# Kernel tuning notes

Measured on AMD Instinct MI355X. Metric: run time of the kernel, lower is better.

## Reference

```python
import jax, jax.numpy as jnp
import numpy as np

B, N, DIM = 1024, 256, 64
NFP, L = 10000, 3
EPS = 1e-6


def layer_norm(x, g, b):
    mu = jnp.mean(x, axis=-1, keepdims=True)
    var = jnp.mean(jnp.square(x - mu), axis=-1, keepdims=True)
    return (x - mu) * jax.lax.rsqrt(var + EPS) * g + b


def setup_inputs() -> dict:
    key = jax.random.key(0)
    ks = jax.random.split(key, 12)
    fingerprints = jax.random.randint(ks[0], (B, N), 0, NFP)
    # sparse-ish symmetric 0/1 adjacency mask (float, as in torch .mul)
    a = (jax.random.uniform(ks[1], (B, N, N)) < 0.05).astype(jnp.float32)
    adjacencies = jnp.maximum(a, jnp.swapaxes(a, 1, 2))
    molecular_sizes = jax.random.randint(ks[2], (B,), 1, N + 1)
    s = 0.02
    word_emb = jax.random.normal(ks[3], (NFP, DIM), jnp.float32) * s
    pos_emb = jax.random.normal(ks[4], (N, DIM), jnp.float32) * s
    emb_ln_g = jnp.ones((DIM,), jnp.float32)
    emb_ln_b = jnp.zeros((DIM,), jnp.float32)
    W1 = jax.random.normal(ks[5], (L, DIM, DIM), jnp.float32) * s
    b1 = jnp.zeros((L, DIM), jnp.float32)
    W2 = jax.random.normal(ks[6], (L, DIM, DIM), jnp.float32) * s
    b2 = jnp.zeros((L, DIM), jnp.float32)
    W3 = jax.random.normal(ks[7], (L, DIM, DIM), jnp.float32) * s
    b3 = jnp.zeros((L, DIM), jnp.float32)
    ln_g = jnp.ones((DIM,), jnp.float32)
    ln_b = jnp.zeros((DIM,), jnp.float32)
    return {"fingerprints": fingerprints, "adjacencies": adjacencies,
            "molecular_sizes": molecular_sizes, "word_emb": word_emb,
            "pos_emb": pos_emb, "emb_ln_g": emb_ln_g, "emb_ln_b": emb_ln_b,
            "W1": W1, "b1": b1, "W2": W2, "b2": b2, "W3": W3, "b3": b3,
            "ln_g": ln_g, "ln_b": ln_b}


def reference(fingerprints, adjacencies, molecular_sizes, word_emb, pos_emb,
              emb_ln_g, emb_ln_b, W1, b1, W2, b2, W3, b3, ln_g, ln_b):
    # demb: word + position embedding, LayerNorm (dropout = identity in eval)
    xs = word_emb[fingerprints] + pos_emb[None, :, :]        # [B, N, D]
    xs = layer_norm(xs, emb_ln_g, emb_ln_b)
    for l in range(L):
        hs1 = jax.nn.relu(jnp.einsum('bnd,ed->bne', xs, W1[l]) + b1[l])
        hs2 = jax.nn.relu(jnp.einsum('bnd,ed->bne', xs, W2[l]) + b2[l])
        attn = jnp.einsum('bnd,bmd->bnm', hs1, hs2) * adjacencies  # masked QK^T, no softmax
        hs3 = jax.nn.relu(jnp.einsum('bnd,ed->bne', xs, W3[l]) + b3[l])
        xs = xs + layer_norm(jnp.einsum('bnm,bmd->bnd', attn, hs3), ln_g, ln_b)
    return xs
```

## Files before the change

kernel.cpp:

```cpp
#include <hip/hip_runtime.h>


#define NB   1024
#define NN   256
#define DD   64
#define NLAY 3

typedef __attribute__((ext_vector_type(8))) short s16x8;
typedef __attribute__((ext_vector_type(4))) short s16x4;
typedef __attribute__((ext_vector_type(4))) float f32x4;

static __device__ __forceinline__ short f2bf(float x) {
    union { float f; unsigned u; } v; v.f = x;
    unsigned r = v.u + 0x7FFFu + ((v.u >> 16) & 1u);
    return (short)(r >> 16);
}

#define MFMA(a, bb, acc) __builtin_amdgcn_mfma_f32_16x16x32_bf16((a), (bb), (acc), 0, 0, 0)

#define STAGE_STRIP(arr)                                                      \
    do {                                                                      \
        _Pragma("unroll") for (int tr_ = 0; tr_ < 2; ++tr_)                   \
        _Pragma("unroll") for (int et_ = 0; et_ < 4; ++et_)                   \
        _Pragma("unroll") for (int r_ = 0; r_ < 4; ++r_)                      \
            hs2s[n0 + tr_*16 + g*4 + r_][et_*16 + c] = f2bf(arr[tr_][et_][r_]); \
    } while (0)

#define READ_AFRAG(dst)                                                       \
    do {                                                                      \
        _Pragma("unroll") for (int tr_ = 0; tr_ < 2; ++tr_)                   \
        _Pragma("unroll") for (int kb_ = 0; kb_ < 2; ++kb_)                   \
            dst[tr_][kb_] = *(const s16x8*)&hs2s[n0 + tr_*16 + c][kb_*32 + g*8]; \
    } while (0)

__global__ __launch_bounds__(512, 2)
void mgnn_fused(const int* __restrict__ fpr, const float* __restrict__ adj,
                const float* __restrict__ wemb, const float* __restrict__ pemb,
                const float* __restrict__ egp, const float* __restrict__ ebp,
                const float* __restrict__ W1p, const float* __restrict__ b1p,
                const float* __restrict__ W2p, const float* __restrict__ b2p,
                const float* __restrict__ W3p, const float* __restrict__ b3p,
                const float* __restrict__ lngp, const float* __restrict__ lnbp,
                float* __restrict__ out)
{
    __shared__ __align__(16) short hs2s[NN][72];
    __shared__ __align__(16) short hs3Ts[DD][264];

    const int b    = blockIdx.x;
    const int tid  = threadIdx.x;
    const int w    = tid >> 6;
    const int lane = tid & 63;
    const int g    = lane >> 4;
    const int c    = lane & 15;
    const int n0   = w * 32;

    const float* __restrict__ adjB = adj + (size_t)b * NN * NN;

    f32x4 xsC[2][4];
    #pragma unroll
    for (int tr = 0; tr < 2; ++tr) {
        const int n = n0 + tr*16 + c;
        const int f = fpr[b*NN + n];
        f32x4 v[4];
        float s1 = 0.f, s2 = 0.f;
        #pragma unroll
        for (int dc = 0; dc < 4; ++dc) {
            const f32x4 wv = *(const f32x4*)&wemb[f*DD + dc*16 + g*4];
            const f32x4 pe = *(const f32x4*)&pemb[n*DD + dc*16 + g*4];
            f32x4 t;
            #pragma unroll
            for (int r = 0; r < 4; ++r) {
                t[r] = wv[r] + pe[r]; s1 += t[r]; s2 += t[r]*t[r];
            }
            v[dc] = t;
        }
        s1 += __shfl_xor(s1, 16); s2 += __shfl_xor(s2, 16);
        s1 += __shfl_xor(s1, 32); s2 += __shfl_xor(s2, 32);
        const float mu  = s1 * 0.015625f;
        const float var = s2 * 0.015625f - mu*mu;
        const float rs  = rsqrtf(var + 1e-6f);
        #pragma unroll
        for (int dc = 0; dc < 4; ++dc) {
            const f32x4 eg = *(const f32x4*)&egp[dc*16 + g*4];
            const f32x4 eb = *(const f32x4*)&ebp[dc*16 + g*4];
            #pragma unroll
            for (int r = 0; r < 4; ++r)
                xsC[tr][dc][r] = (v[dc][r] - mu) * rs * eg[r] + eb[r];
        }
    }

    auto stageXS = [&]() {
        #pragma unroll
        for (int tr = 0; tr < 2; ++tr)
            #pragma unroll
            for (int dc = 0; dc < 4; ++dc) {
                s16x4 pk;
                #pragma unroll
                for (int r = 0; r < 4; ++r) pk[r] = f2bf(xsC[tr][dc][r]);
                *(s16x4*)&hs2s[n0 + tr*16 + c][dc*16 + g*4] = pk;
            }
    };

    s16x8 xsf[2][2];
    stageXS();
    __syncthreads();
    READ_AFRAG(xsf);

    float hsv[2][4][4];

    auto gemmHs = [&](const float* __restrict__ Wm, const float* __restrict__ bm) {
        s16x8 wf[4][2];
        #pragma unroll
        for (int et = 0; et < 4; ++et) {
            const float* p = Wm + (et*16 + c)*DD + g*8;
            #pragma unroll
            for (int kb = 0; kb < 2; ++kb) {
                s16x8 v;
                #pragma unroll
                for (int j = 0; j < 8; ++j) v[j] = f2bf(p[kb*32 + j]);
                wf[et][kb] = v;
            }
        }
        #pragma unroll
        for (int tr = 0; tr < 2; ++tr) {
            #pragma unroll
            for (int et = 0; et < 4; ++et) {
                f32x4 acc = {0.f, 0.f, 0.f, 0.f};
                acc = MFMA(xsf[tr][0], wf[et][0], acc);
                acc = MFMA(xsf[tr][1], wf[et][1], acc);
                const float bv = bm[et*16 + c];
                #pragma unroll
                for (int r = 0; r < 4; ++r)
                    hsv[tr][et][r] = fmaxf(acc[r] + bv, 0.f);
            }
        }
    };

    #pragma unroll 1
    for (int l = 0; l < NLAY; ++l) {
        gemmHs(W1p + l*DD*DD, b1p + l*DD);
        STAGE_STRIP(hsv);
        __syncthreads();
        s16x8 h1f[2][2];
        READ_AFRAG(h1f);

        gemmHs(W2p + l*DD*DD, b2p + l*DD);
        STAGE_STRIP(hsv);

        gemmHs(W3p + l*DD*DD, b3p + l*DD);
        #pragma unroll
        for (int tr = 0; tr < 2; ++tr) {
            #pragma unroll
            for (int et = 0; et < 4; ++et) {
                s16x4 pk;
                #pragma unroll
                for (int r = 0; r < 4; ++r) pk[r] = f2bf(hsv[tr][et][r]);
                *(s16x4*)&hs3Ts[et*16 + c][n0 + tr*16 + g*4] = pk;
            }
        }
        __syncthreads();

        f32x4 pv[2][4];
        {
            const f32x4 z4 = {0.f, 0.f, 0.f, 0.f};
            #pragma unroll
            for (int tr = 0; tr < 2; ++tr)
                #pragma unroll
                for (int dc = 0; dc < 4; ++dc) pv[tr][dc] = z4;
        }

        #pragma unroll 1
        for (int cc = 0; cc < 8; ++cc) {
            float amT[2][2][4];
            #pragma unroll
            for (int tr = 0; tr < 2; ++tr)
                #pragma unroll
                for (int mc = 0; mc < 2; ++mc)
                    #pragma unroll
                    for (int r = 0; r < 4; ++r)
                        amT[tr][mc][r] =
                            adjB[(size_t)(cc*32 + mc*16 + g*4 + r)*NN + n0 + tr*16 + c];

            s16x8 a2[2][2];
            #pragma unroll
            for (int mc = 0; mc < 2; ++mc)
                #pragma unroll
                for (int kb = 0; kb < 2; ++kb)
                    a2[mc][kb] = *(const s16x8*)&hs2s[cc*32 + mc*16 + c][kb*32 + g*8];

            s16x8 h3f[4];
            #pragma unroll
            for (int dc = 0; dc < 4; ++dc)
                h3f[dc] = *(const s16x8*)&hs3Ts[dc*16 + c][cc*32 + g*8];

            float smv[2][2][4];
            #pragma unroll
            for (int tr = 0; tr < 2; ++tr) {
                #pragma unroll
                for (int mc = 0; mc < 2; ++mc) {
                    f32x4 st = {0.f, 0.f, 0.f, 0.f};
                    st = MFMA(a2[mc][0], h1f[tr][0], st);
                    st = MFMA(a2[mc][1], h1f[tr][1], st);
                    #pragma unroll
                    for (int r = 0; r < 4; ++r)
                        smv[tr][mc][r] = st[r] * amT[tr][mc][r];
                }
            }

            #pragma unroll
            for (int tr = 0; tr < 2; ++tr) {
                s16x8 pb;
                #pragma unroll
                for (int j = 0; j < 8; ++j) {
                    const int srcl = ((2*(g & 1) + (j >> 2)) << 4) | c;
                    const float v0 = __shfl(smv[tr][0][j & 3], srcl);
                    const float v1 = __shfl(smv[tr][1][j & 3], srcl);
                    pb[j] = f2bf((g & 2) ? v1 : v0);
                }
                #pragma unroll
                for (int dc = 0; dc < 4; ++dc)
                    pv[tr][dc] = MFMA(h3f[dc], pb, pv[tr][dc]);
            }
        }

        #pragma unroll
        for (int tr = 0; tr < 2; ++tr) {
            float s1 = 0.f, s2 = 0.f;
            #pragma unroll
            for (int dc = 0; dc < 4; ++dc)
                #pragma unroll
                for (int r = 0; r < 4; ++r) {
                    const float x = pv[tr][dc][r];
                    s1 += x; s2 += x*x;
                }
            s1 += __shfl_xor(s1, 16); s2 += __shfl_xor(s2, 16);
            s1 += __shfl_xor(s1, 32); s2 += __shfl_xor(s2, 32);
            const float mu  = s1 * 0.015625f;
            const float var = s2 * 0.015625f - mu*mu;
            const float rs  = rsqrtf(var + 1e-6f);
            #pragma unroll
            for (int dc = 0; dc < 4; ++dc) {
                const f32x4 lg = *(const f32x4*)&lngp[dc*16 + g*4];
                const f32x4 lb = *(const f32x4*)&lnbp[dc*16 + g*4];
                #pragma unroll
                for (int r = 0; r < 4; ++r)
                    xsC[tr][dc][r] += (pv[tr][dc][r] - mu) * rs * lg[r] + lb[r];
            }
        }

        if (l < NLAY - 1) {
            __syncthreads();
            stageXS();
            __syncthreads();
            READ_AFRAG(xsf);
        }
    }

    const size_t ob = (size_t)b * NN * DD;
    #pragma unroll
    for (int tr = 0; tr < 2; ++tr) {
        const int n = n0 + tr*16 + c;
        #pragma unroll
        for (int dc = 0; dc < 4; ++dc)
            *(f32x4*)&out[ob + (size_t)n*DD + dc*16 + g*4] = xsC[tr][dc];
    }
}

extern "C" void kernel_launch(void* const* d_in, const int* in_sizes, int n_in,
                              void* d_out, int out_size, void* d_ws, size_t ws_size,
                              hipStream_t stream) {
    const int*   fpr  = (const int*)  d_in[0];
    const float* adj  = (const float*)d_in[1];
    const float* wemb = (const float*)d_in[3];
    const float* pemb = (const float*)d_in[4];
    const float* eg   = (const float*)d_in[5];
    const float* eb   = (const float*)d_in[6];
    const float* W1   = (const float*)d_in[7];
    const float* b1   = (const float*)d_in[8];
    const float* W2   = (const float*)d_in[9];
    const float* b2   = (const float*)d_in[10];
    const float* W3   = (const float*)d_in[11];
    const float* b3   = (const float*)d_in[12];
    const float* lng  = (const float*)d_in[13];
    const float* lnb  = (const float*)d_in[14];

    mgnn_fused<<<dim3(NB), dim3(512), 0, stream>>>(
        fpr, adj, wemb, pemb, eg, eb, W1, b1, W2, b2, W3, b3, lng, lnb,
        (float*)d_out);
}
```

Before: 312.9 us.

## Load adjacency once into LDS bitmasks and reuse across all layers

Reads the fp32 adjacency for each molecule once at kernel start with double-buffered loads, compresses it via wave ballots into 64-bit bitmasks in shared memory, and applies the mask from LDS in every layer instead of re-reading global memory three times. This cuts global traffic for the dominant input. It adds about 8 KB of LDS per block and assumes the adjacency is a 0/1 mask. It also switches LDS accesses to memcpy helpers and adds compiler memory barriers.

```diff
diff --git a/kernel.cpp b/kernel.cpp
--- a/kernel.cpp
+++ b/kernel.cpp
@@ -14,6 +14,13 @@
     union { float f; unsigned u; } v; v.f = x;
     unsigned r = v.u + 0x7FFFu + ((v.u >> 16) & 1u);
     return (short)(r >> 16);
+}
+
+static __device__ __forceinline__ s16x8 lds_read8(const short* p) {
+    s16x8 v; __builtin_memcpy(&v, p, 16); return v;
+}
+static __device__ __forceinline__ void lds_write4(short* p, s16x4 v) {
+    __builtin_memcpy(p, &v, 8);
 }
 
 #define MFMA(a, bb, acc) __builtin_amdgcn_mfma_f32_16x16x32_bf16((a), (bb), (acc), 0, 0, 0)
@@ -30,7 +37,28 @@
     do {                                                                      \
         _Pragma("unroll") for (int tr_ = 0; tr_ < 2; ++tr_)                   \
         _Pragma("unroll") for (int kb_ = 0; kb_ < 2; ++kb_)                   \
-            dst[tr_][kb_] = *(const s16x8*)&hs2s[n0 + tr_*16 + c][kb_*32 + g*8]; \
+            dst[tr_][kb_] = lds_read8(&hs2s[n0 + tr_*16 + c][kb_*32 + g*8]);  \
+    } while (0)
+
+#define LOADA(cc, am)                                                         \
+    do {                                                                      \
+        _Pragma("unroll") for (int tr_ = 0; tr_ < 2; ++tr_)                   \
+        _Pragma("unroll") for (int mc_ = 0; mc_ < 2; ++mc_)                   \
+        _Pragma("unroll") for (int r_ = 0; r_ < 4; ++r_)                      \
+            am[tr_][mc_][r_] = adjB[(size_t)((cc)*32 + mc_*16 + g*4 + r_)*NN + n0 + tr_*16 + c]; \
+    } while (0)
+
+#define PACKB(cc, am)                                                         \
+    do {                                                                      \
+        unsigned long long bbuf_[16];                                         \
+        _Pragma("unroll") for (int tr_ = 0; tr_ < 2; ++tr_)                   \
+        _Pragma("unroll") for (int mc_ = 0; mc_ < 2; ++mc_)                   \
+        _Pragma("unroll") for (int r_ = 0; r_ < 4; ++r_)                      \
+            bbuf_[(tr_*2 + mc_)*4 + r_] = __ballot(am[tr_][mc_][r_] != 0.f);  \
+        if (lane == 0) {                                                      \
+            _Pragma("unroll") for (int i_ = 0; i_ < 16; ++i_)                 \
+                adjbits[w][cc][i_] = bbuf_[i_];                               \
+        }                                                                     \
     } while (0)
 
 __global__ __launch_bounds__(512, 2)
@@ -45,6 +73,7 @@
 {
     __shared__ __align__(16) short hs2s[NN][72];
     __shared__ __align__(16) short hs3Ts[DD][264];
+    __shared__ unsigned long long adjbits[8][8][16];
 
     const int b    = blockIdx.x;
     const int tid  = threadIdx.x;
@@ -97,7 +126,7 @@
                 s16x4 pk;
                 #pragma unroll
                 for (int r = 0; r < 4; ++r) pk[r] = f2bf(xsC[tr][dc][r]);
-                *(s16x4*)&hs2s[n0 + tr*16 + c][dc*16 + g*4] = pk;
+                lds_write4(&hs2s[n0 + tr*16 + c][dc*16 + g*4], pk);
             }
     };
 
@@ -105,6 +134,19 @@
     stageXS();
     __syncthreads();
     READ_AFRAG(xsf);
+    asm volatile("" ::: "memory");
+
+    {
+        float amA[2][2][4], amB[2][2][4];
+        LOADA(0, amA);
+        #pragma unroll 1
+        for (int cc = 0; cc < 8; cc += 2) {
+            LOADA(cc + 1, amB);
+            PACKB(cc, amA);
+            if (cc + 2 < 8) LOADA(cc + 2, amA);
+            PACKB(cc + 1, amB);
+        }
+    }
 
     float hsv[2][4][4];
 
@@ -143,6 +185,7 @@
         __syncthreads();
         s16x8 h1f[2][2];
         READ_AFRAG(h1f);
+        asm volatile("" ::: "memory");
 
         gemmHs(W2p + l*DD*DD, b2p + l*DD);
         STAGE_STRIP(hsv);
@@ -155,7 +198,7 @@
                 s16x4 pk;
                 #pragma unroll
                 for (int r = 0; r < 4; ++r) pk[r] = f2bf(hsv[tr][et][r]);
-                *(s16x4*)&hs3Ts[et*16 + c][n0 + tr*16 + g*4] = pk;
+                lds_write4(&hs3Ts[et*16 + c][n0 + tr*16 + g*4], pk);
             }
         }
         __syncthreads();
@@ -171,27 +214,17 @@
 
         #pragma unroll 1
         for (int cc = 0; cc < 8; ++cc) {
-            float amT[2][2][4];
-            #pragma unroll
-            for (int tr = 0; tr < 2; ++tr)
-                #pragma unroll
-                for (int mc = 0; mc < 2; ++mc)
-                    #pragma unroll
-                    for (int r = 0; r < 4; ++r)
-                        amT[tr][mc][r] =
-                            adjB[(size_t)(cc*32 + mc*16 + g*4 + r)*NN + n0 + tr*16 + c];
-
             s16x8 a2[2][2];
             #pragma unroll
             for (int mc = 0; mc < 2; ++mc)
                 #pragma unroll
                 for (int kb = 0; kb < 2; ++kb)
-                    a2[mc][kb] = *(const s16x8*)&hs2s[cc*32 + mc*16 + c][kb*32 + g*8];
+                    a2[mc][kb] = lds_read8(&hs2s[cc*32 + mc*16 + c][kb*32 + g*8]);
 
             s16x8 h3f[4];
             #pragma unroll
             for (int dc = 0; dc < 4; ++dc)
-                h3f[dc] = *(const s16x8*)&hs3Ts[dc*16 + c][cc*32 + g*8];
+                h3f[dc] = lds_read8(&hs3Ts[dc*16 + c][cc*32 + g*8]);
 
             float smv[2][2][4];
             #pragma unroll
@@ -202,8 +235,11 @@
                     st = MFMA(a2[mc][0], h1f[tr][0], st);
                     st = MFMA(a2[mc][1], h1f[tr][1], st);
                     #pragma unroll
-                    for (int r = 0; r < 4; ++r)
-                        smv[tr][mc][r] = st[r] * amT[tr][mc][r];
+                    for (int r = 0; r < 4; ++r) {
+                        const unsigned long long wv =
+                            adjbits[w][cc][(tr*2 + mc)*4 + r];
+                        smv[tr][mc][r] = ((wv >> lane) & 1ull) ? st[r] : 0.f;
+                    }
                 }
             }
 
@@ -241,10 +277,10 @@
             #pragma unroll
             for (int dc = 0; dc < 4; ++dc) {
                 const f32x4 lg = *(const f32x4*)&lngp[dc*16 + g*4];
-                const f32x4 lb = *(const f32x4*)&lnbp[dc*16 + g*4];
+                const f32x4 lb4 = *(const f32x4*)&lnbp[dc*16 + g*4];
                 #pragma unroll
                 for (int r = 0; r < 4; ++r)
-                    xsC[tr][dc][r] += (pv[tr][dc][r] - mu) * rs * lg[r] + lb[r];
+                    xsC[tr][dc][r] += (pv[tr][dc][r] - mu) * rs * lg[r] + lb4[r];
             }
         }
 
@@ -253,6 +289,7 @@
             stageXS();
             __syncthreads();
             READ_AFRAG(xsf);
+            asm volatile("" ::: "memory");
         }
     }
 
```

After: 347.9 us. 1.11x slower.
